# Kernel optimization log

Measured on AMD Instinct MI355X. Metric: run time of the kernel, lower is better.

The kernel has to match this reference:

```python
import jax, jax.numpy as jnp
import numpy as np

B, S, H, KV, D = 1, 2048, 16, 4, 128
HID = H * D
CACHE = 2048
EPS = 1e-6
SCALE = 128 ** -0.5  # query_pre_attn_scalar ** -0.5
NEG = -1e9


def setup_inputs() -> dict:
    key = jax.random.key(0)
    ks = jax.random.split(key, 12)
    hidden_states = jax.random.normal(ks[0], (B, S, HID), jnp.float32)
    # rotary embeddings (Gemma3 style, base 10000, half-dim frequencies)
    pos = jnp.arange(S, dtype=jnp.float32)[:, None]
    inv_freq = 1.0 / (10000.0 ** (jnp.arange(0, D, 2, dtype=jnp.float32) / D))
    freqs = pos * inv_freq[None, :]
    emb = jnp.concatenate([freqs, freqs], axis=-1)  # [S, D]
    cos = jnp.cos(emb)[None]  # [1, S, D]
    sin = jnp.sin(emb)[None]
    # additive causal mask [B, 1, S, S]
    r = jnp.arange(S)
    attention_mask = jnp.where(r[:, None] >= r[None, :], 0.0, NEG).astype(jnp.float32)[None, None]
    lyra_key_cache = jax.random.normal(ks[1], (1, KV, CACHE, D), jnp.float32)
    lyra_value_cache = jax.random.normal(ks[2], (1, KV, CACHE, D), jnp.float32)
    w = 0.02
    Wq = jax.random.normal(ks[3], (H * D, HID), jnp.float32) * w
    Wk = jax.random.normal(ks[4], (KV * D, HID), jnp.float32) * w
    Wv = jax.random.normal(ks[5], (KV * D, HID), jnp.float32) * w
    Wo = jax.random.normal(ks[6], (HID, H * D), jnp.float32) * w
    q_norm_w = jax.random.normal(ks[7], (D,), jnp.float32) * 0.1
    k_norm_w = jax.random.normal(ks[8], (D,), jnp.float32) * 0.1
    return dict(hidden_states=hidden_states, cos=cos, sin=sin,
                attention_mask=attention_mask,
                lyra_key_cache=lyra_key_cache, lyra_value_cache=lyra_value_cache,
                Wq=Wq, Wk=Wk, Wv=Wv, Wo=Wo, q_norm_w=q_norm_w, k_norm_w=k_norm_w)


def _rmsnorm(x, w):
    xf = x.astype(jnp.float32)
    n = xf * jax.lax.rsqrt(jnp.mean(xf * xf, axis=-1, keepdims=True) + EPS)
    return (n * (1.0 + w.astype(jnp.float32))).astype(x.dtype)


def _rotate_half(x):
    h = x.shape[-1] // 2
    return jnp.concatenate([-x[..., h:], x[..., :h]], axis=-1)


def _rope(x, c, s):
    return x * c + _rotate_half(x) * s


def _attend(q, k, v, mask, n_rep):
    # q: [B,h,Sq,D]; k,v: [B,KV,Sk,D]; mask additive float broadcastable to [B,h,Sq,Sk]
    k = jnp.repeat(k, n_rep, axis=1)
    v = jnp.repeat(v, n_rep, axis=1)
    w = jnp.einsum('bhqd,bhkd->bhqk', q, k) * SCALE + mask
    w = jax.nn.softmax(w.astype(jnp.float32), axis=-1).astype(q.dtype)
    out = jnp.einsum('bhqk,bhkd->bhqd', w, v)
    return out, w


def reference(hidden_states, cos, sin, attention_mask, lyra_key_cache,
              lyra_value_cache, Wq, Wk, Wv, Wo, q_norm_w, k_norm_w):
    bsz, q_len, _ = hidden_states.shape
    q = (hidden_states @ Wq.T).reshape(bsz, q_len, H, D).transpose(0, 2, 1, 3)
    k = (hidden_states @ Wk.T).reshape(bsz, q_len, KV, D).transpose(0, 2, 1, 3)
    v = (hidden_states @ Wv.T).reshape(bsz, q_len, KV, D).transpose(0, 2, 1, 3)
    q = _rmsnorm(q, q_norm_w)
    k = _rmsnorm(k, k_norm_w)
    vanilla_q, lyra_q = q[:, :H // 2], q[:, H // 2:]
    c = cos[:, None]  # [B,1,S,D]
    s = sin[:, None]
    n_rep = (H // 2) // KV  # stream_num_key_value_groups
    # vanilla stream
    vanilla_q_rope = _rope(vanilla_q, c, s)
    k_rope = _rope(k, c, s)
    vanilla_out, vanilla_w = _attend(vanilla_q_rope, k_rope, v, attention_mask, n_rep)
    # lyra stream: prepend static KV cache; bool mask added as float (faithful to source)
    lyra_q_rope = _rope(lyra_q, c, s)
    lk = jnp.concatenate([jnp.broadcast_to(lyra_key_cache, (bsz, KV, CACHE, D)), k_rope], axis=2)
    lv = jnp.concatenate([jnp.broadcast_to(lyra_value_cache, (bsz, KV, CACHE, D)), v], axis=2)
    rows = jnp.arange(q_len)[:, None]
    cols = jnp.arange(CACHE + q_len)[None, :]
    lyra_mask = (rows < cols - CACHE).astype(jnp.float32)[None, None]  # True -> +1.0, as in torch code
    lyra_out, _ = _attend(lyra_q_rope, lk, lv, lyra_mask, n_rep)
    combined = jnp.concatenate([vanilla_out, lyra_out], axis=1)  # [B,H,S,D]
    combined = combined.transpose(0, 2, 1, 3).reshape(bsz, q_len, H * D)
    attn_output = combined @ Wo.T
    return attn_output, vanilla_w
```

## Files before the change

### kernel.cpp

```cpp
#include <hip/hip_runtime.h>
#include <math.h>

#define S_LEN 2048
#define HID 2048
#define NH 16
#define NKV 4
#define DH 128
#define CACHE_LEN 2048
#define QKV_W 3072
#define SCALE 0.08838834764831845f
#define EPS 1e-6f
#define LYRA_C 12.0f

typedef short bf16x8 __attribute__((ext_vector_type(8)));
typedef float f32x4 __attribute__((ext_vector_type(4)));

static __device__ __forceinline__ short f2bf(float x) {
  union { float f; unsigned u; } v; v.f = x;
  unsigned r = (v.u + 0x7FFF + ((v.u >> 16) & 1)) >> 16;
  return (short)r;
}

#define GLDS16(g, l)                                                      \
  __builtin_amdgcn_global_load_lds(                                       \
      (const __attribute__((address_space(1))) unsigned int*)(g),         \
      (__attribute__((address_space(3))) unsigned int*)(l), 16, 0, 0)

__global__ __launch_bounds__(256) void pack_bf16(
    const float* __restrict__ src, short* __restrict__ dst) {
  const int i = (blockIdx.x * 256 + threadIdx.x) * 8;
  float4 a = *(const float4*)(src + i);
  float4 b = *(const float4*)(src + i + 4);
  bf16x8 o;
  o[0] = f2bf(a.x); o[1] = f2bf(a.y); o[2] = f2bf(a.z); o[3] = f2bf(a.w);
  o[4] = f2bf(b.x); o[5] = f2bf(b.y); o[6] = f2bf(b.z); o[7] = f2bf(b.w);
  *(bf16x8*)(dst + i) = o;
}

__global__ __launch_bounds__(256) void gemm_bf16(
    const short* __restrict__ A, const short* __restrict__ B,
    float* __restrict__ C, int K, int ldc) {
  __shared__ short sA[4096];
  __shared__ short sB[4096];
  const int t = threadIdx.x;
  const int w = t >> 6;
  const int lane = t & 63;
  const int quad = lane >> 4;
  const int l16 = lane & 15;
  const int tm = blockIdx.y * 128;
  const int tn = blockIdx.x * 128;
  const int srow = lane >> 2;
  const int scol = (lane & 3) * 8;
  const int mblk = (w & 1) * 64;
  const int nblk = (w >> 1) * 64;
  f32x4 acc[4][4];
#pragma unroll
  for (int i = 0; i < 4; ++i)
#pragma unroll
    for (int j = 0; j < 4; ++j) acc[i][j] = (f32x4){0.f, 0.f, 0.f, 0.f};

  const short* Ab = A + (size_t)(tm + w * 32 + srow) * K + scol;
  const short* Bb = B + (size_t)(tn + w * 32 + srow) * K + scol;
  const size_t rstep = (size_t)16 * K;

  for (int k0 = 0; k0 < K; k0 += 32) {
    GLDS16(Ab + k0, sA + (w * 2 + 0) * 512);
    GLDS16(Ab + rstep + k0, sA + (w * 2 + 1) * 512);
    GLDS16(Bb + k0, sB + (w * 2 + 0) * 512);
    GLDS16(Bb + rstep + k0, sB + (w * 2 + 1) * 512);
    __syncthreads();
    bf16x8 af[4], bfv[4];
#pragma unroll
    for (int ms = 0; ms < 4; ++ms)
      af[ms] = *(const bf16x8*)&sA[(mblk + ms * 16 + l16) * 32 + quad * 8];
#pragma unroll
    for (int ns = 0; ns < 4; ++ns)
      bfv[ns] = *(const bf16x8*)&sB[(nblk + ns * 16 + l16) * 32 + quad * 8];
#pragma unroll
    for (int ms = 0; ms < 4; ++ms)
#pragma unroll
      for (int ns = 0; ns < 4; ++ns)
        acc[ms][ns] = __builtin_amdgcn_mfma_f32_16x16x32_bf16(
            af[ms], bfv[ns], acc[ms][ns], 0, 0, 0);
    __syncthreads();
  }
#pragma unroll
  for (int ms = 0; ms < 4; ++ms)
#pragma unroll
    for (int ns = 0; ns < 4; ++ns) {
      const int row = tm + mblk + ms * 16 + quad * 4;
      const int col = tn + nblk + ns * 16 + l16;
#pragma unroll
      for (int r = 0; r < 4; ++r)
        C[(size_t)(row + r) * ldc + col] = acc[ms][ns][r];
    }
}

__global__ __launch_bounds__(256) void rms_rope(
    float* __restrict__ qkv,
    const float* __restrict__ cosb, const float* __restrict__ sinb,
    const float* __restrict__ qw, const float* __restrict__ kw) {
  const int unit = blockIdx.x * 4 + (threadIdx.x >> 6);
  const int lane = threadIdx.x & 63;
  const int total_q = S_LEN * NH;
  float* base;
  const float* w;
  int pos;
  if (unit < total_q) {
    pos = unit >> 4;
    int head = unit & 15;
    base = qkv + (size_t)pos * QKV_W + head * DH;
    w = qw;
  } else {
    int u = unit - total_q;
    pos = u >> 2;
    int head = u & 3;
    base = qkv + (size_t)pos * QKV_W + 2048 + head * DH;
    w = kw;
  }
  float x0 = base[lane];
  float x1 = base[lane + 64];
  float ss = x0 * x0 + x1 * x1;
#pragma unroll
  for (int off = 32; off > 0; off >>= 1) ss += __shfl_xor(ss, off);
  float r = rsqrtf(ss * (1.0f / 128.0f) + EPS);
  float n0 = x0 * r * (1.0f + w[lane]);
  float n1 = x1 * r * (1.0f + w[lane + 64]);
  float c0 = cosb[(size_t)pos * DH + lane];
  float c1 = cosb[(size_t)pos * DH + lane + 64];
  float s0 = sinb[(size_t)pos * DH + lane];
  float s1 = sinb[(size_t)pos * DH + lane + 64];
  base[lane]      = n0 * c0 - n1 * s0;
  base[lane + 64] = n1 * c1 + n0 * s1;
}

__global__ __launch_bounds__(256) void pack_k(
    const float* __restrict__ qkv, const float* __restrict__ kcache,
    short* __restrict__ Kbf) {
  const int idx = blockIdx.x * 256 + threadIdx.x;
  const int e4 = idx * 4;
  const int kvh = e4 >> 19;
  const int rem = e4 & ((1 << 19) - 1);
  const int key = rem >> 7;
  const int d = rem & 127;
  float4 v;
  if (key < CACHE_LEN)
    v = *(const float4*)(kcache + (((size_t)kvh * CACHE_LEN + key) << 7) + d);
  else
    v = *(const float4*)(qkv + (size_t)(key - CACHE_LEN) * QKV_W + 2048 + kvh * DH + d);
  short4 o;
  o.x = f2bf(v.x); o.y = f2bf(v.y); o.z = f2bf(v.z); o.w = f2bf(v.w);
  const int dsw = d ^ ((key & 7) << 3);
  *(short4*)(Kbf + (size_t)(e4 - d) + dsw) = o;
}

__global__ __launch_bounds__(256) void pack_vt(
    const float* __restrict__ qkv, const float* __restrict__ vcache,
    short* __restrict__ Vt) {
  __shared__ float tile[64][65];
  const int key0 = blockIdx.x * 64;
  const int d0 = blockIdx.y * 64;
  const int kvh = blockIdx.z;
  const int t = threadIdx.x;
  const int c = t & 63;
  const int r0 = t >> 6;
#pragma unroll
  for (int i = 0; i < 16; ++i) {
    int r = r0 + i * 4;
    int key = key0 + r;
    float v;
    if (key < CACHE_LEN)
      v = vcache[(((size_t)kvh * CACHE_LEN + key) << 7) + d0 + c];
    else
      v = qkv[(size_t)(key - CACHE_LEN) * QKV_W + 2560 + kvh * DH + d0 + c];
    tile[r][c] = v;
  }
  __syncthreads();
#pragma unroll
  for (int i = 0; i < 16; ++i) {
    int wr = r0 + i * 4;
    int csw = c ^ (((d0 + wr) & 7) << 3);
    Vt[((size_t)kvh * DH + d0 + wr) * 4096 + key0 + csw] = f2bf(tile[c][wr]);
  }
}

__global__ __launch_bounds__(256) void vscore_gemm(
    const float* __restrict__ qkv, float* __restrict__ wout) {
  const int bx = blockIdx.x, by = blockIdx.y, h = blockIdx.z;
  if (bx > by) return;
  __shared__ float As[8][132];
  __shared__ float Bs[8][132];
  const int t = threadIdx.x;
  const int lr = t >> 1;
  const int lc = (t & 1) * 4;
  const float* Ap = qkv + h * DH + (size_t)(by * 128 + lr) * QKV_W + lc;
  const float* Bp = qkv + 2048 + (h >> 1) * DH + (size_t)(bx * 128 + lr) * QKV_W + lc;
  const int tx = t & 15;
  const int ty = t >> 4;
  float acc[8][8];
#pragma unroll
  for (int i = 0; i < 8; ++i)
#pragma unroll
    for (int j = 0; j < 8; ++j) acc[i][j] = 0.f;
  for (int k0 = 0; k0 < DH; k0 += 8) {
    float4 av = *(const float4*)(Ap + k0);
    float4 bv = *(const float4*)(Bp + k0);
    __syncthreads();
    As[lc + 0][lr] = av.x; As[lc + 1][lr] = av.y;
    As[lc + 2][lr] = av.z; As[lc + 3][lr] = av.w;
    Bs[lc + 0][lr] = bv.x; Bs[lc + 1][lr] = bv.y;
    Bs[lc + 2][lr] = bv.z; Bs[lc + 3][lr] = bv.w;
    __syncthreads();
#pragma unroll
    for (int k = 0; k < 8; ++k) {
      float4 a0 = *(const float4*)&As[k][ty * 4];
      float4 a1 = *(const float4*)&As[k][64 + ty * 4];
      float4 b0 = *(const float4*)&Bs[k][tx * 4];
      float4 b1 = *(const float4*)&Bs[k][64 + tx * 4];
      float ar[8] = {a0.x, a0.y, a0.z, a0.w, a1.x, a1.y, a1.z, a1.w};
      float br[8] = {b0.x, b0.y, b0.z, b0.w, b1.x, b1.y, b1.z, b1.w};
#pragma unroll
      for (int i = 0; i < 8; ++i)
#pragma unroll
        for (int j = 0; j < 8; ++j)
          acc[i][j] = fmaf(ar[i], br[j], acc[i][j]);
    }
  }
  float* Ch = wout + (size_t)h * S_LEN * S_LEN;
#pragma unroll
  for (int ih = 0; ih < 2; ++ih)
#pragma unroll
    for (int i = 0; i < 4; ++i) {
      int row = by * 128 + ih * 64 + ty * 4 + i;
      int ai = ih * 4 + i;
      float* Crow = Ch + (size_t)row * S_LEN + bx * 128;
      *(float4*)(Crow + tx * 4) =
          make_float4(acc[ai][0] * SCALE, acc[ai][1] * SCALE,
                      acc[ai][2] * SCALE, acc[ai][3] * SCALE);
      *(float4*)(Crow + 64 + tx * 4) =
          make_float4(acc[ai][4] * SCALE, acc[ai][5] * SCALE,
                      acc[ai][6] * SCALE, acc[ai][7] * SCALE);
    }
}

__global__ __launch_bounds__(256) void vsoftmax(float* __restrict__ wout) {
  const int row = blockIdx.x;
  const int h = blockIdx.y;
  float* p = wout + (size_t)h * S_LEN * S_LEN + (size_t)row * S_LEN;
  const int n = row + 1;
  const int t = threadIdx.x;
  const int lane = t & 63, wid = t >> 6;
  __shared__ float red[4];
  float x[8];
#pragma unroll
  for (int i = 0; i < 8; ++i) {
    int j = t + i * 256;
    x[i] = (j < n) ? p[j] : -INFINITY;
  }
  float m = -INFINITY;
#pragma unroll
  for (int i = 0; i < 8; ++i) m = fmaxf(m, x[i]);
#pragma unroll
  for (int off = 32; off > 0; off >>= 1) m = fmaxf(m, __shfl_xor(m, off));
  if (lane == 0) red[wid] = m;
  __syncthreads();
  m = fmaxf(fmaxf(red[0], red[1]), fmaxf(red[2], red[3]));
  __syncthreads();
  float l = 0.f;
#pragma unroll
  for (int i = 0; i < 8; ++i) {
    x[i] = expf(x[i] - m);
    l += x[i];
  }
#pragma unroll
  for (int off = 32; off > 0; off >>= 1) l += __shfl_xor(l, off);
  if (lane == 0) red[wid] = l;
  __syncthreads();
  l = (red[0] + red[1]) + (red[2] + red[3]);
  const float inv = 1.0f / l;
#pragma unroll
  for (int i = 0; i < 8; ++i) {
    int j = t + i * 256;
    if (j < n) p[j] = x[i] * inv;
  }
  for (int j = n + t; j < S_LEN; j += 256) p[j] = 0.f;
}

__global__ __launch_bounds__(64) void vout_mfma(
    const float* __restrict__ wout, const short* __restrict__ Vtb,
    short* __restrict__ combined_bf) {
  const int qt = blockIdx.x;
  const int h = blockIdx.y;
  const int kvh = h >> 1;
  const int lane = threadIdx.x;
  const int quad = lane >> 4;
  const int l16 = lane & 15;
  const int row0 = qt * 16;
  const int swx = (l16 & 7) << 3;
  const float* Wr =
      wout + (size_t)h * S_LEN * S_LEN + (size_t)(row0 + l16) * S_LEN + quad * 8;
  const short* Vb = Vtb + (size_t)kvh * DH * 4096 + 2048;
  f32x4 acc[8];
#pragma unroll
  for (int i = 0; i < 8; ++i) acc[i] = (f32x4){0.f, 0.f, 0.f, 0.f};
  const int kend = row0 + 16;
  for (int k0 = 0; k0 < kend; k0 += 32) {
    float4 a0 = *(const float4*)(Wr + k0);
    float4 a1 = *(const float4*)(Wr + k0 + 4);
    bf16x8 af;
    af[0] = f2bf(a0.x); af[1] = f2bf(a0.y); af[2] = f2bf(a0.z); af[3] = f2bf(a0.w);
    af[4] = f2bf(a1.x); af[5] = f2bf(a1.y); af[6] = f2bf(a1.z); af[7] = f2bf(a1.w);
#pragma unroll
    for (int t8 = 0; t8 < 8; ++t8) {
      bf16x8 bv = *(const bf16x8*)(
          Vb + (size_t)(t8 * 16 + l16) * 4096 + ((k0 + quad * 8) ^ swx));
      acc[t8] = __builtin_amdgcn_mfma_f32_16x16x32_bf16(af, bv, acc[t8], 0, 0, 0);
    }
  }
  const int rbase = row0 + quad * 4;
#pragma unroll
  for (int t8 = 0; t8 < 8; ++t8)
#pragma unroll
    for (int r = 0; r < 4; ++r)
      combined_bf[(size_t)(rbase + r) * HID + h * DH + t8 * 16 + l16] =
          f2bf(acc[t8][r]);
}

static __device__ __forceinline__ void stage_kv(
    const short* Kb, const short* Vb, short* buf, int key0, int w, int lane) {
#pragma unroll
  for (int i = 0; i < 2; ++i)
    GLDS16(Kb + ((size_t)key0 + w * 8 + i * 4) * 128 + lane * 8,
           buf + (w * 8 + i * 4) * 128);
#pragma unroll
  for (int j = 0; j < 2; ++j)
    GLDS16(Vb + (size_t)(w * 16 + j * 8 + (lane >> 3)) * 4096 + key0 +
               (lane & 7) * 8,
           buf + 8192 + (w * 16 + j * 8) * 64);
}

__global__ __launch_bounds__(512) void lyra_attn(
    const float* __restrict__ qkv,
    const short* __restrict__ Kbf,
    const short* __restrict__ Vtb,
    short* __restrict__ combined_bf) {
  __shared__ short sKV[3][16384];
  __shared__ short sP[8][16][64];
  __shared__ float sL[64];
  const int hj = blockIdx.x;
  const int qt = blockIdx.y;
  const int kvh = hj >> 1;
  const int t = threadIdx.x;
  const int w = t >> 6;
  const int lane = t & 63;
  const int quad = lane >> 4;
  const int l16 = lane & 15;
  const int wr = w >> 1;
  const int wc = w & 1;
  const int row0 = qt * 64;
  const int rbase = row0 + wr * 16 + quad * 4;
  const int swx = (l16 & 7) << 4;

  bf16x8 qf[4];
  {
    const float* qrow =
        qkv + (size_t)(row0 + wr * 16 + l16) * QKV_W + (8 + hj) * DH;
#pragma unroll
    for (int ks = 0; ks < 4; ++ks) {
      float4 f0 = *(const float4*)(qrow + ks * 32 + quad * 8);
      float4 f1 = *(const float4*)(qrow + ks * 32 + quad * 8 + 4);
      qf[ks][0] = f2bf(f0.x); qf[ks][1] = f2bf(f0.y);
      qf[ks][2] = f2bf(f0.z); qf[ks][3] = f2bf(f0.w);
      qf[ks][4] = f2bf(f1.x); qf[ks][5] = f2bf(f1.y);
      qf[ks][6] = f2bf(f1.z); qf[ks][7] = f2bf(f1.w);
    }
  }
  bf16x8 onesf;
#pragma unroll
  for (int i = 0; i < 8; ++i) onesf[i] = (short)0x3F80;

  f32x4 accO[8];
#pragma unroll
  for (int i = 0; i < 8; ++i) accO[i] = (f32x4){0.f, 0.f, 0.f, 0.f};
  f32x4 accL = (f32x4){0.f, 0.f, 0.f, 0.f};

  const short* Kb = Kbf + (size_t)kvh * 4096 * DH;
  const short* Vb = Vtb + (size_t)kvh * DH * 4096;

  stage_kv(Kb, Vb, &sKV[0][0], 0, w, lane);
  stage_kv(Kb, Vb, &sKV[1][0], 64, w, lane);

  short* sPw = &sP[w][0][0];
  int b = 0;
  for (int kt = 0; kt < 64; ++kt) {
    asm volatile("s_waitcnt vmcnt(4)" ::: "memory");
    __builtin_amdgcn_s_barrier();
    __builtin_amdgcn_sched_barrier(0);

    {
      int nb = b + 2; if (nb >= 3) nb -= 3;
      stage_kv(Kb, Vb, &sKV[nb][0], ((kt + 2) & 63) * 64, w, lane);
    }

    const char* Ksc = (const char*)&sKV[b][0];
    const char* Vsc = (const char*)&sKV[b][8192];

    f32x4 accS[2];
#pragma unroll
    for (int s = 0; s < 2; ++s) accS[s] = (f32x4){0.f, 0.f, 0.f, 0.f};
    __builtin_amdgcn_s_setprio(1);
#pragma unroll
    for (int s = 0; s < 2; ++s) {
      const char* krow = Ksc + (wc * 32 + s * 16 + l16) * 256;
#pragma unroll
      for (int ks = 0; ks < 4; ++ks) {
        bf16x8 bk = *(const bf16x8*)(krow + ((ks * 64 + quad * 16) ^ swx));
        accS[s] = __builtin_amdgcn_mfma_f32_16x16x32_bf16(qf[ks], bk, accS[s],
                                                          0, 0, 0);
      }
    }
    __builtin_amdgcn_s_setprio(0);

    const int base = kt * 64 + wc * 32;
    if (kt >= 32) {
#pragma unroll
      for (int s = 0; s < 2; ++s) {
        const int col = base + s * 16 + l16;
#pragma unroll
        for (int r = 0; r < 4; ++r) {
          const int row = quad * 4 + r;
          float sc = accS[s][r] * SCALE;
          if ((col - CACHE_LEN) > (rbase + r)) sc += 1.0f;
          const int sl = (s * 2 + (l16 >> 3)) ^ (row & 7);
          sPw[row * 64 + sl * 8 + (l16 & 7)] = f2bf(__expf(sc - LYRA_C));
        }
      }
    } else {
#pragma unroll
      for (int s = 0; s < 2; ++s)
#pragma unroll
        for (int r = 0; r < 4; ++r) {
          const int row = quad * 4 + r;
          const int sl = (s * 2 + (l16 >> 3)) ^ (row & 7);
          sPw[row * 64 + sl * 8 + (l16 & 7)] =
              f2bf(__expf(accS[s][r] * SCALE - LYRA_C));
        }
    }

    __builtin_amdgcn_s_setprio(1);
    bf16x8 ap = *(const bf16x8*)&sPw[l16 * 64 + ((quad ^ (l16 & 7)) << 3)];
    accL = __builtin_amdgcn_mfma_f32_16x16x32_bf16(ap, onesf, accL, 0, 0, 0);
#pragma unroll
    for (int t8 = 0; t8 < 8; ++t8) {
      bf16x8 bv = *(const bf16x8*)(
          Vsc + (t8 * 16 + l16) * 128 + ((wc * 64 + quad * 16) ^ swx));
      accO[t8] = __builtin_amdgcn_mfma_f32_16x16x32_bf16(ap, bv, accO[t8],
                                                         0, 0, 0);
    }
    __builtin_amdgcn_s_setprio(0);

    ++b; if (b == 3) b = 0;
  }

  __syncthreads();
  float* sO = (float*)&sKV[0][0];
  if (wc == 1) {
#pragma unroll
    for (int t8 = 0; t8 < 8; ++t8)
#pragma unroll
      for (int r = 0; r < 4; ++r)
        sO[((wr * 16 + quad * 4 + r) << 7) + t8 * 16 + l16] = accO[t8][r];
    if (l16 == 0) {
#pragma unroll
      for (int r = 0; r < 4; ++r) sL[wr * 16 + quad * 4 + r] = accL[r];
    }
  }
  __syncthreads();
  if (wc == 0) {
    float linv[4];
#pragma unroll
    for (int r = 0; r < 4; ++r)
      linv[r] = 1.0f / (accL[r] + sL[wr * 16 + quad * 4 + r]);
#pragma unroll
    for (int t8 = 0; t8 < 8; ++t8)
#pragma unroll
      for (int r = 0; r < 4; ++r) {
        float o = accO[t8][r] + sO[((wr * 16 + quad * 4 + r) << 7) + t8 * 16 + l16];
        combined_bf[(size_t)(rbase + r) * HID + (8 + hj) * DH + t8 * 16 + l16] =
            f2bf(o * linv[r]);
      }
  }
}

extern "C" void kernel_launch(void* const* d_in, const int* in_sizes, int n_in,
                              void* d_out, int out_size, void* d_ws, size_t ws_size,
                              hipStream_t stream) {
  (void)in_sizes; (void)n_in; (void)out_size; (void)ws_size;
  const float* hidden = (const float*)d_in[0];
  const float* cosb   = (const float*)d_in[1];
  const float* sinb   = (const float*)d_in[2];
  const float* kcache = (const float*)d_in[4];
  const float* vcache = (const float*)d_in[5];
  const float* Wq = (const float*)d_in[6];
  const float* Wk = (const float*)d_in[7];
  const float* Wv = (const float*)d_in[8];
  const float* Wo = (const float*)d_in[9];
  const float* qw = (const float*)d_in[10];
  const float* kw = (const float*)d_in[11];

  float* out  = (float*)d_out;
  float* wout = out + (size_t)4194304;

  float* qkv = (float*)d_ws;
  short* Kbf = (short*)(qkv + (size_t)2048 * QKV_W);
  short* Vtb = Kbf + (size_t)4 * 4096 * DH;
  short* combined_bf = Vtb + (size_t)4 * DH * 4096;
  short* Wo_bf = combined_bf + (size_t)2048 * HID;

  short* hidden_bf = (short*)wout;
  short* Wqkv_bf = hidden_bf + (size_t)2048 * HID;

  pack_bf16<<<dim3(2048), 256, 0, stream>>>(hidden, hidden_bf);
  pack_bf16<<<dim3(2048), 256, 0, stream>>>(Wq, Wqkv_bf);
  pack_bf16<<<dim3(512), 256, 0, stream>>>(Wk, Wqkv_bf + (size_t)2048 * 2048);
  pack_bf16<<<dim3(512), 256, 0, stream>>>(Wv, Wqkv_bf + (size_t)2560 * 2048);
  pack_bf16<<<dim3(2048), 256, 0, stream>>>(Wo, Wo_bf);

  gemm_bf16<<<dim3(24, 16), 256, 0, stream>>>(hidden_bf, Wqkv_bf, qkv, 2048, QKV_W);
  rms_rope<<<dim3(10240), 256, 0, stream>>>(qkv, cosb, sinb, qw, kw);
  pack_k<<<dim3(2048), 256, 0, stream>>>(qkv, kcache, Kbf);
  pack_vt<<<dim3(64, 2, 4), 256, 0, stream>>>(qkv, vcache, Vtb);
  lyra_attn<<<dim3(8, 32), 512, 0, stream>>>(qkv, Kbf, Vtb, combined_bf);
  vscore_gemm<<<dim3(16, 16, 8), 256, 0, stream>>>(qkv, wout);
  vsoftmax<<<dim3(2048, 8), 256, 0, stream>>>(wout);
  vout_mfma<<<dim3(128, 8), 64, 0, stream>>>(wout, Vtb, combined_bf);
  gemm_bf16<<<dim3(16, 16), 256, 0, stream>>>(combined_bf, Wo_bf, out, 2048, HID);
}
```

Before: 579.4 us.

## Fuse vanilla attention scores, softmax and PV into one MFMA kernel

Replaces the FP32 SIMT score GEMM, the separate softmax pass and the PV kernel with a single flash-style MFMA kernel. It computes QK^T with split bf16 hi/lo terms (three MFMAs) to keep near-FP32 accuracy, uses a fixed exponent offset instead of a running max, and writes unnormalized probabilities. A light vnorm pass then rescales the weights by a stored inverse row sum. This removes the slow FP32 GEMM and one full read/write of the 128MB weight tensor. The cost is extra K-low packing and a risk of overflow or underflow from the fixed LYRA_C offset.

Result: faster. 513.0 us (-11.5%).

```diff
diff --git a/kernel.cpp b/kernel.cpp
--- a/kernel.cpp
+++ b/kernel.cpp
@@ -19,6 +19,12 @@
   union { float f; unsigned u; } v; v.f = x;
   unsigned r = (v.u + 0x7FFF + ((v.u >> 16) & 1)) >> 16;
   return (short)r;
+}
+
+static __device__ __forceinline__ float bf2f(short h) {
+  union { unsigned u; float f; } v;
+  v.u = ((unsigned)(unsigned short)h) << 16;
+  return v.f;
 }
 
 #define GLDS16(g, l)                                                      \
@@ -136,22 +142,31 @@
 
 __global__ __launch_bounds__(256) void pack_k(
     const float* __restrict__ qkv, const float* __restrict__ kcache,
-    short* __restrict__ Kbf) {
+    short* __restrict__ Kbf, short* __restrict__ Klo) {
   const int idx = blockIdx.x * 256 + threadIdx.x;
   const int e4 = idx * 4;
   const int kvh = e4 >> 19;
   const int rem = e4 & ((1 << 19) - 1);
   const int key = rem >> 7;
   const int d = rem & 127;
-  float4 v;
-  if (key < CACHE_LEN)
-    v = *(const float4*)(kcache + (((size_t)kvh * CACHE_LEN + key) << 7) + d);
-  else
-    v = *(const float4*)(qkv + (size_t)(key - CACHE_LEN) * QKV_W + 2048 + kvh * DH + d);
-  short4 o;
-  o.x = f2bf(v.x); o.y = f2bf(v.y); o.z = f2bf(v.z); o.w = f2bf(v.w);
   const int dsw = d ^ ((key & 7) << 3);
-  *(short4*)(Kbf + (size_t)(e4 - d) + dsw) = o;
+  if (key < CACHE_LEN) {
+    float4 v = *(const float4*)(kcache + (((size_t)kvh * CACHE_LEN + key) << 7) + d);
+    short4 o;
+    o.x = f2bf(v.x); o.y = f2bf(v.y); o.z = f2bf(v.z); o.w = f2bf(v.w);
+    *(short4*)(Kbf + (size_t)(e4 - d) + dsw) = o;
+  } else {
+    float4 v = *(const float4*)(qkv + (size_t)(key - CACHE_LEN) * QKV_W + 2048 + kvh * DH + d);
+    short4 o;
+    o.x = f2bf(v.x); o.y = f2bf(v.y); o.z = f2bf(v.z); o.w = f2bf(v.w);
+    *(short4*)(Kbf + (size_t)(e4 - d) + dsw) = o;
+    short4 ol;
+    ol.x = f2bf(v.x - bf2f(o.x));
+    ol.y = f2bf(v.y - bf2f(o.y));
+    ol.z = f2bf(v.z - bf2f(o.z));
+    ol.w = f2bf(v.w - bf2f(o.w));
+    *(short4*)(Klo + ((size_t)kvh * 2048 + (key - CACHE_LEN)) * 128 + dsw) = ol;
+  }
 }
 
 __global__ __launch_bounds__(256) void pack_vt(
@@ -182,148 +197,6 @@
     int csw = c ^ (((d0 + wr) & 7) << 3);
     Vt[((size_t)kvh * DH + d0 + wr) * 4096 + key0 + csw] = f2bf(tile[c][wr]);
   }
-}
-
-__global__ __launch_bounds__(256) void vscore_gemm(
-    const float* __restrict__ qkv, float* __restrict__ wout) {
-  const int bx = blockIdx.x, by = blockIdx.y, h = blockIdx.z;
-  if (bx > by) return;
-  __shared__ float As[8][132];
-  __shared__ float Bs[8][132];
-  const int t = threadIdx.x;
-  const int lr = t >> 1;
-  const int lc = (t & 1) * 4;
-  const float* Ap = qkv + h * DH + (size_t)(by * 128 + lr) * QKV_W + lc;
-  const float* Bp = qkv + 2048 + (h >> 1) * DH + (size_t)(bx * 128 + lr) * QKV_W + lc;
-  const int tx = t & 15;
-  const int ty = t >> 4;
-  float acc[8][8];
-#pragma unroll
-  for (int i = 0; i < 8; ++i)
-#pragma unroll
-    for (int j = 0; j < 8; ++j) acc[i][j] = 0.f;
-  for (int k0 = 0; k0 < DH; k0 += 8) {
-    float4 av = *(const float4*)(Ap + k0);
-    float4 bv = *(const float4*)(Bp + k0);
-    __syncthreads();
-    As[lc + 0][lr] = av.x; As[lc + 1][lr] = av.y;
-    As[lc + 2][lr] = av.z; As[lc + 3][lr] = av.w;
-    Bs[lc + 0][lr] = bv.x; Bs[lc + 1][lr] = bv.y;
-    Bs[lc + 2][lr] = bv.z; Bs[lc + 3][lr] = bv.w;
-    __syncthreads();
-#pragma unroll
-    for (int k = 0; k < 8; ++k) {
-      float4 a0 = *(const float4*)&As[k][ty * 4];
-      float4 a1 = *(const float4*)&As[k][64 + ty * 4];
-      float4 b0 = *(const float4*)&Bs[k][tx * 4];
-      float4 b1 = *(const float4*)&Bs[k][64 + tx * 4];
-      float ar[8] = {a0.x, a0.y, a0.z, a0.w, a1.x, a1.y, a1.z, a1.w};
-      float br[8] = {b0.x, b0.y, b0.z, b0.w, b1.x, b1.y, b1.z, b1.w};
-#pragma unroll
-      for (int i = 0; i < 8; ++i)
-#pragma unroll
-        for (int j = 0; j < 8; ++j)
-          acc[i][j] = fmaf(ar[i], br[j], acc[i][j]);
-    }
-  }
-  float* Ch = wout + (size_t)h * S_LEN * S_LEN;
-#pragma unroll
-  for (int ih = 0; ih < 2; ++ih)
-#pragma unroll
-    for (int i = 0; i < 4; ++i) {
-      int row = by * 128 + ih * 64 + ty * 4 + i;
-      int ai = ih * 4 + i;
-      float* Crow = Ch + (size_t)row * S_LEN + bx * 128;
-      *(float4*)(Crow + tx * 4) =
-          make_float4(acc[ai][0] * SCALE, acc[ai][1] * SCALE,
-                      acc[ai][2] * SCALE, acc[ai][3] * SCALE);
-      *(float4*)(Crow + 64 + tx * 4) =
-          make_float4(acc[ai][4] * SCALE, acc[ai][5] * SCALE,
-                      acc[ai][6] * SCALE, acc[ai][7] * SCALE);
-    }
-}
-
-__global__ __launch_bounds__(256) void vsoftmax(float* __restrict__ wout) {
-  const int row = blockIdx.x;
-  const int h = blockIdx.y;
-  float* p = wout + (size_t)h * S_LEN * S_LEN + (size_t)row * S_LEN;
-  const int n = row + 1;
-  const int t = threadIdx.x;
-  const int lane = t & 63, wid = t >> 6;
-  __shared__ float red[4];
-  float x[8];
-#pragma unroll
-  for (int i = 0; i < 8; ++i) {
-    int j = t + i * 256;
-    x[i] = (j < n) ? p[j] : -INFINITY;
-  }
-  float m = -INFINITY;
-#pragma unroll
-  for (int i = 0; i < 8; ++i) m = fmaxf(m, x[i]);
-#pragma unroll
-  for (int off = 32; off > 0; off >>= 1) m = fmaxf(m, __shfl_xor(m, off));
-  if (lane == 0) red[wid] = m;
-  __syncthreads();
-  m = fmaxf(fmaxf(red[0], red[1]), fmaxf(red[2], red[3]));
-  __syncthreads();
-  float l = 0.f;
-#pragma unroll
-  for (int i = 0; i < 8; ++i) {
-    x[i] = expf(x[i] - m);
-    l += x[i];
-  }
-#pragma unroll
-  for (int off = 32; off > 0; off >>= 1) l += __shfl_xor(l, off);
-  if (lane == 0) red[wid] = l;
-  __syncthreads();
-  l = (red[0] + red[1]) + (red[2] + red[3]);
-  const float inv = 1.0f / l;
-#pragma unroll
-  for (int i = 0; i < 8; ++i) {
-    int j = t + i * 256;
-    if (j < n) p[j] = x[i] * inv;
-  }
-  for (int j = n + t; j < S_LEN; j += 256) p[j] = 0.f;
-}
-
-__global__ __launch_bounds__(64) void vout_mfma(
-    const float* __restrict__ wout, const short* __restrict__ Vtb,
-    short* __restrict__ combined_bf) {
-  const int qt = blockIdx.x;
-  const int h = blockIdx.y;
-  const int kvh = h >> 1;
-  const int lane = threadIdx.x;
-  const int quad = lane >> 4;
-  const int l16 = lane & 15;
-  const int row0 = qt * 16;
-  const int swx = (l16 & 7) << 3;
-  const float* Wr =
-      wout + (size_t)h * S_LEN * S_LEN + (size_t)(row0 + l16) * S_LEN + quad * 8;
-  const short* Vb = Vtb + (size_t)kvh * DH * 4096 + 2048;
-  f32x4 acc[8];
-#pragma unroll
-  for (int i = 0; i < 8; ++i) acc[i] = (f32x4){0.f, 0.f, 0.f, 0.f};
-  const int kend = row0 + 16;
-  for (int k0 = 0; k0 < kend; k0 += 32) {
-    float4 a0 = *(const float4*)(Wr + k0);
-    float4 a1 = *(const float4*)(Wr + k0 + 4);
-    bf16x8 af;
-    af[0] = f2bf(a0.x); af[1] = f2bf(a0.y); af[2] = f2bf(a0.z); af[3] = f2bf(a0.w);
-    af[4] = f2bf(a1.x); af[5] = f2bf(a1.y); af[6] = f2bf(a1.z); af[7] = f2bf(a1.w);
-#pragma unroll
-    for (int t8 = 0; t8 < 8; ++t8) {
-      bf16x8 bv = *(const bf16x8*)(
-          Vb + (size_t)(t8 * 16 + l16) * 4096 + ((k0 + quad * 8) ^ swx));
-      acc[t8] = __builtin_amdgcn_mfma_f32_16x16x32_bf16(af, bv, acc[t8], 0, 0, 0);
-    }
-  }
-  const int rbase = row0 + quad * 4;
-#pragma unroll
-  for (int t8 = 0; t8 < 8; ++t8)
-#pragma unroll
-    for (int r = 0; r < 4; ++r)
-      combined_bf[(size_t)(rbase + r) * HID + h * DH + t8 * 16 + l16] =
-          f2bf(acc[t8][r]);
 }
 
 static __device__ __forceinline__ void stage_kv(
@@ -492,6 +365,213 @@
   }
 }
 
+static __device__ __forceinline__ void stage_van(
+    const short* Kh, const short* Kl, const short* Vb, short* buf,
+    int key0, int w, int lane) {
+#pragma unroll
+  for (int i = 0; i < 2; ++i) {
+    GLDS16(Kh + ((size_t)key0 + w * 8 + i * 4) * 128 + lane * 8,
+           buf + (w * 8 + i * 4) * 128);
+    GLDS16(Kl + ((size_t)key0 + w * 8 + i * 4) * 128 + lane * 8,
+           buf + 8192 + (w * 8 + i * 4) * 128);
+  }
+#pragma unroll
+  for (int j = 0; j < 2; ++j)
+    GLDS16(Vb + (size_t)(w * 16 + j * 8 + (lane >> 3)) * 4096 + key0 +
+               (lane & 7) * 8,
+           buf + 16384 + (w * 16 + j * 8) * 64);
+}
+
+__global__ __launch_bounds__(512) void vanilla_attn(
+    const float* __restrict__ qkv,
+    const short* __restrict__ Kbf,
+    const short* __restrict__ Klo,
+    const short* __restrict__ Vtb,
+    float* __restrict__ wout,
+    float* __restrict__ vinv,
+    short* __restrict__ combined_bf) {
+  __shared__ short sKV[2][24576];
+  __shared__ short sP[8][16][64];
+  __shared__ float sL[64];
+  const int hj = blockIdx.x;
+  const int qt = blockIdx.y;
+  const int kvh = hj >> 1;
+  const int t = threadIdx.x;
+  const int w = t >> 6;
+  const int lane = t & 63;
+  const int quad = lane >> 4;
+  const int l16 = lane & 15;
+  const int wr = w >> 1;
+  const int wc = w & 1;
+  const int row0 = qt * 64;
+  const int rbase = row0 + wr * 16 + quad * 4;
+  const int swx = (l16 & 7) << 4;
+
+  bf16x8 qh[4], ql[4];
+  {
+    const float* qrow =
+        qkv + (size_t)(row0 + wr * 16 + l16) * QKV_W + hj * DH;
+#pragma unroll
+    for (int ks = 0; ks < 4; ++ks) {
+#pragma unroll
+      for (int e = 0; e < 8; ++e) {
+        float x = qrow[ks * 32 + quad * 8 + e];
+        short h = f2bf(x);
+        qh[ks][e] = h;
+        ql[ks][e] = f2bf(x - bf2f(h));
+      }
+    }
+  }
+
+  f32x4 accO[8];
+#pragma unroll
+  for (int i = 0; i < 8; ++i) accO[i] = (f32x4){0.f, 0.f, 0.f, 0.f};
+  float accR[4] = {0.f, 0.f, 0.f, 0.f};
+
+  const short* Kh = Kbf + ((size_t)kvh * 4096 + 2048) * DH;
+  const short* Kl = Klo + (size_t)kvh * 2048 * DH;
+  const short* Vb = Vtb + (size_t)kvh * DH * 4096 + 2048;
+  float* wrow = wout + (size_t)hj * S_LEN * S_LEN;
+
+  stage_van(Kh, Kl, Vb, &sKV[0][0], 0, w, lane);
+
+  short* sPw = &sP[w][0][0];
+  int b = 0;
+  for (int kt = 0; kt <= qt; ++kt) {
+    asm volatile("s_waitcnt vmcnt(0)" ::: "memory");
+    __builtin_amdgcn_s_barrier();
+    __builtin_amdgcn_sched_barrier(0);
+
+    if (kt < qt)
+      stage_van(Kh, Kl, Vb, &sKV[b ^ 1][0], (kt + 1) * 64, w, lane);
+
+    const char* Khs = (const char*)&sKV[b][0];
+    const char* Kls = (const char*)&sKV[b][8192];
+    const char* Vsc = (const char*)&sKV[b][16384];
+
+    f32x4 accS[2];
+#pragma unroll
+    for (int s = 0; s < 2; ++s) accS[s] = (f32x4){0.f, 0.f, 0.f, 0.f};
+    __builtin_amdgcn_s_setprio(1);
+#pragma unroll
+    for (int s = 0; s < 2; ++s) {
+      const char* krh = Khs + (wc * 32 + s * 16 + l16) * 256;
+      const char* krl = Kls + (wc * 32 + s * 16 + l16) * 256;
+#pragma unroll
+      for (int ks = 0; ks < 4; ++ks) {
+        const int off = (ks * 64 + quad * 16) ^ swx;
+        bf16x8 kh = *(const bf16x8*)(krh + off);
+        bf16x8 kl = *(const bf16x8*)(krl + off);
+        accS[s] = __builtin_amdgcn_mfma_f32_16x16x32_bf16(qh[ks], kh, accS[s], 0, 0, 0);
+        accS[s] = __builtin_amdgcn_mfma_f32_16x16x32_bf16(ql[ks], kh, accS[s], 0, 0, 0);
+        accS[s] = __builtin_amdgcn_mfma_f32_16x16x32_bf16(qh[ks], kl, accS[s], 0, 0, 0);
+      }
+    }
+    __builtin_amdgcn_s_setprio(0);
+
+    const int key0 = kt * 64;
+    const bool diag = (kt == qt);
+    float pr[4] = {0.f, 0.f, 0.f, 0.f};
+#pragma unroll
+    for (int s = 0; s < 2; ++s) {
+      const int col = key0 + wc * 32 + s * 16 + l16;
+#pragma unroll
+      for (int r = 0; r < 4; ++r) {
+        const int row = quad * 4 + r;
+        const int grow = rbase + r;
+        float p = __expf(accS[s][r] * SCALE - LYRA_C);
+        if (diag && col > grow) p = 0.f;
+        pr[r] += p;
+        const int sl = (s * 2 + (l16 >> 3)) ^ (row & 7);
+        sPw[row * 64 + sl * 8 + (l16 & 7)] = f2bf(p);
+        wrow[(size_t)grow * S_LEN + col] = p;
+      }
+    }
+#pragma unroll
+    for (int r = 0; r < 4; ++r) {
+      float v = pr[r];
+      v += __shfl_xor(v, 1);
+      v += __shfl_xor(v, 2);
+      v += __shfl_xor(v, 4);
+      v += __shfl_xor(v, 8);
+      accR[r] += v;
+    }
+
+    __builtin_amdgcn_s_setprio(1);
+    bf16x8 ap = *(const bf16x8*)&sPw[l16 * 64 + ((quad ^ (l16 & 7)) << 3)];
+#pragma unroll
+    for (int t8 = 0; t8 < 8; ++t8) {
+      bf16x8 bv = *(const bf16x8*)(
+          Vsc + (t8 * 16 + l16) * 128 + ((wc * 64 + quad * 16) ^ swx));
+      accO[t8] = __builtin_amdgcn_mfma_f32_16x16x32_bf16(ap, bv, accO[t8],
+                                                         0, 0, 0);
+    }
+    __builtin_amdgcn_s_setprio(0);
+
+    b ^= 1;
+  }
+
+  __syncthreads();
+  float* sO = (float*)&sKV[0][0];
+  if (wc == 1) {
+#pragma unroll
+    for (int t8 = 0; t8 < 8; ++t8)
+#pragma unroll
+      for (int r = 0; r < 4; ++r)
+        sO[((wr * 16 + quad * 4 + r) << 7) + t8 * 16 + l16] = accO[t8][r];
+    if (l16 == 0) {
+#pragma unroll
+      for (int r = 0; r < 4; ++r) sL[wr * 16 + quad * 4 + r] = accR[r];
+    }
+  }
+  __syncthreads();
+  if (wc == 0) {
+    float linv[4];
+#pragma unroll
+    for (int r = 0; r < 4; ++r)
+      linv[r] = 1.0f / (accR[r] + sL[wr * 16 + quad * 4 + r]);
+    if (l16 == 0) {
+#pragma unroll
+      for (int r = 0; r < 4; ++r) vinv[hj * S_LEN + rbase + r] = linv[r];
+    }
+#pragma unroll
+    for (int t8 = 0; t8 < 8; ++t8)
+#pragma unroll
+      for (int r = 0; r < 4; ++r) {
+        float o = accO[t8][r] + sO[((wr * 16 + quad * 4 + r) << 7) + t8 * 16 + l16];
+        combined_bf[(size_t)(rbase + r) * HID + hj * DH + t8 * 16 + l16] =
+            f2bf(o * linv[r]);
+      }
+  }
+}
+
+__global__ __launch_bounds__(256) void vnorm(
+    const float* __restrict__ vinv, float* __restrict__ wout) {
+  const int row = blockIdx.x;
+  const int h = blockIdx.y;
+  float* p = wout + (size_t)h * S_LEN * S_LEN + (size_t)row * S_LEN;
+  const float inv = vinv[h * S_LEN + row];
+  const int t = threadIdx.x;
+#pragma unroll
+  for (int i = 0; i < 2; ++i) {
+    const int j = (t + i * 256) * 4;
+    float4 v;
+    if (j > row) {
+      v = make_float4(0.f, 0.f, 0.f, 0.f);
+    } else if (j + 3 <= row) {
+      v = *(const float4*)(p + j);
+      v.x *= inv; v.y *= inv; v.z *= inv; v.w *= inv;
+    } else {
+      v = *(const float4*)(p + j);
+      v.x = (j + 0 <= row) ? v.x * inv : 0.f;
+      v.y = (j + 1 <= row) ? v.y * inv : 0.f;
+      v.z = (j + 2 <= row) ? v.z * inv : 0.f;
+      v.w = (j + 3 <= row) ? v.w * inv : 0.f;
+    }
+    *(float4*)(p + j) = v;
+  }
+}
+
 extern "C" void kernel_launch(void* const* d_in, const int* in_sizes, int n_in,
                               void* d_out, int out_size, void* d_ws, size_t ws_size,
                               hipStream_t stream) {
@@ -520,6 +600,9 @@
   short* hidden_bf = (short*)wout;
   short* Wqkv_bf = hidden_bf + (size_t)2048 * HID;
 
+  short* Klo  = (short*)out;
+  float* vinv = (float*)(Klo + (size_t)4 * 2048 * DH);
+
   pack_bf16<<<dim3(2048), 256, 0, stream>>>(hidden, hidden_bf);
   pack_bf16<<<dim3(2048), 256, 0, stream>>>(Wq, Wqkv_bf);
   pack_bf16<<<dim3(512), 256, 0, stream>>>(Wk, Wqkv_bf + (size_t)2048 * 2048);
@@ -528,11 +611,11 @@
 
   gemm_bf16<<<dim3(24, 16), 256, 0, stream>>>(hidden_bf, Wqkv_bf, qkv, 2048, QKV_W);
   rms_rope<<<dim3(10240), 256, 0, stream>>>(qkv, cosb, sinb, qw, kw);
-  pack_k<<<dim3(2048), 256, 0, stream>>>(qkv, kcache, Kbf);
+  pack_k<<<dim3(2048), 256, 0, stream>>>(qkv, kcache, Kbf, Klo);
   pack_vt<<<dim3(64, 2, 4), 256, 0, stream>>>(qkv, vcache, Vtb);
   lyra_attn<<<dim3(8, 32), 512, 0, stream>>>(qkv, Kbf, Vtb, combined_bf);
-  vscore_gemm<<<dim3(16, 16, 8), 256, 0, stream>>>(qkv, wout);
-  vsoftmax<<<dim3(2048, 8), 256, 0, stream>>>(wout);
-  vout_mfma<<<dim3(128, 8), 64, 0, stream>>>(wout, Vtb, combined_bf);
+  vanilla_attn<<<dim3(8, 32), 512, 0, stream>>>(qkv, Kbf, Klo, Vtb, wout, vinv,
+                                                combined_bf);
+  vnorm<<<dim3(2048, 8), 256, 0, stream>>>(vinv, wout);
   gemm_bf16<<<dim3(16, 16), 256, 0, stream>>>(combined_bf, Wo_bf, out, 2048, HID);
 }
```
